# Optimization experiments

Hardware: AMD Instinct MI355X
Metric: run time of the kernel (lower is better)

## Reference

```python
import jax, jax.numpy as jnp
import numpy as np

N = 100000   # nodes
E = 1200000  # edges
D = 64       # feat_dim == num_hidden
G = 64       # graphs in batch
EPS = 1e-5   # BatchNorm eps


def setup_inputs() -> dict:
    key = jax.random.key(0)
    ks = jax.random.split(key, 24)
    inp = {}
    inp['x'] = jax.random.normal(ks[0], (N, D), jnp.float32)
    inp['edge_index'] = jax.random.randint(ks[1], (2, E), 0, N, dtype=jnp.int32)
    inp['batch'] = jnp.sort(jax.random.randint(ks[2], (N,), 0, G, dtype=jnp.int32))
    s = 1.0 / np.sqrt(D)
    for i, kw in zip(range(1, 4), ks[3:6]):
        inp[f'W{i}'] = jax.random.normal(kw, (D, D), jnp.float32) * s
    for i, kb in zip(range(1, 4), ks[6:9]):
        inp[f'b{i}'] = jax.random.normal(kb, (D,), jnp.float32) * 0.02
    for i, base in zip(range(1, 3), (9, 13)):
        inp[f'g{i}'] = 1.0 + 0.1 * jax.random.normal(ks[base], (D,), jnp.float32)
        inp[f'be{i}'] = 0.1 * jax.random.normal(ks[base + 1], (D,), jnp.float32)
        inp[f'rm{i}'] = 0.1 * jax.random.normal(ks[base + 2], (D,), jnp.float32)
        inp[f'rv{i}'] = jax.random.uniform(ks[base + 3], (D,), jnp.float32, 0.5, 1.5)
    return inp


def _gcn_conv(x, W, b, src, dst, n):
    # PyG GCNConv: h = X W; symmetric normalization with self-loops; scatter-add; + bias
    h = x @ W
    deg = jax.ops.segment_sum(jnp.ones((src.shape[0],), h.dtype), dst, num_segments=n) + 1.0
    dis = jax.lax.rsqrt(deg)                          # deg >= 1 from self loop
    msg = (dis[src] * dis[dst])[:, None] * h[src]     # [E, D] gather + normalize
    out = jax.ops.segment_sum(msg, dst, num_segments=n)
    out = out + (dis * dis)[:, None] * h              # self-loop contribution
    return out + b


def _bn(x, g, be, rm, rv):
    # BatchNorm1d in eval mode (running stats)
    return (x - rm) * jax.lax.rsqrt(rv + EPS) * g + be


def reference(x, edge_index, batch, W1, b1, W2, b2, W3, b3,
              g1, be1, rm1, rv1, g2, be2, rm2, rv2):
    src, dst = edge_index[0], edge_index[1]
    h = jax.nn.relu(_bn(_gcn_conv(x, W1, b1, src, dst, N), g1, be1, rm1, rv1))
    h = jax.nn.relu(_bn(_gcn_conv(h, W2, b2, src, dst, N), g2, be2, rm2, rv2))
    h = _gcn_conv(h, W3, b3, src, dst, N)
    # global mean pool over graphs
    counts = jax.ops.segment_sum(jnp.ones((N,), h.dtype), batch, num_segments=G)
    sums = jax.ops.segment_sum(h, batch, num_segments=G)
    hg = sums / jnp.maximum(counts, 1.0)[:, None]
    return (h, hg)
```

## Files before the change

### kernel.cpp

```cpp
#include <hip/hip_runtime.h>
#include <hip/hip_fp16.h>

#define D 64
#define EPS 1e-5f

#define BK_SHIFT 9
#define BK_W 512
#define NBMAX 256
#define BK_CAP 8192
#define CHUNK 4096

typedef _Float16 h8v __attribute__((ext_vector_type(8)));
typedef float f4v __attribute__((ext_vector_type(4)));


__global__ __launch_bounds__(256) void bucket_k(const int* __restrict__ src,
                                                const int* __restrict__ dst,
                                                int* __restrict__ bcnt,
                                                int* __restrict__ pairs,
                                                int e, int nbk) {
  __shared__ int hcnt[NBMAX];
  __shared__ int hbase[NBMAX];
  const int t = threadIdx.x;
  const int e0 = blockIdx.x * CHUNK;
  const int e1 = min(e0 + CHUNK, e);
  for (int i = t; i < nbk; i += 256) hcnt[i] = 0;
  __syncthreads();
  for (int i = e0 + t; i < e1; i += 256)
    atomicAdd(&hcnt[dst[i] >> BK_SHIFT], 1);
  __syncthreads();
  for (int i = t; i < nbk; i += 256) {
    int c = hcnt[i];
    hbase[i] = c ? atomicAdd(&bcnt[i], c) : 0;
    hcnt[i] = 0;
  }
  __syncthreads();
  for (int i = e0 + t; i < e1; i += 256) {
    int s = src[i], d = dst[i];
    int b = d >> BK_SHIFT;
    int r = hbase[b] + atomicAdd(&hcnt[b], 1);
    if (r < BK_CAP) pairs[(size_t)b * BK_CAP + r] = (s << BK_SHIFT) | (d & (BK_W - 1));
  }
}


__global__ __launch_bounds__(256) void bucket2csr_k(const int* __restrict__ bcnt,
                                                    const int* __restrict__ pairs,
                                                    int2* __restrict__ rpdeg,
                                                    float* __restrict__ dis,
                                                    int* __restrict__ col, int n) {
  __shared__ int h[BK_W];
  __shared__ int cur[BK_W];
  __shared__ int s1[256], s2[256];
  __shared__ int stage[BK_CAP];
  const int b = blockIdx.x, t = threadIdx.x;
  const int base = b << BK_SHIFT;
  const int slab0 = b * BK_CAP;
  const int m = min(bcnt[b], BK_CAP);

  h[t] = 0; h[t + 256] = 0;
  for (int i = t; i < BK_CAP; i += 256) stage[i] = 0;
  __syncthreads();
  const int* p = pairs + (size_t)b * BK_CAP;
  for (int i = t; i < m; i += 256) atomicAdd(&h[p[i] & (BK_W - 1)], 1);
  __syncthreads();

  const int pc1 = (h[t] + 3) & ~3;
  const int pc2 = (h[t + 256] + 3) & ~3;
  s1[t] = pc1; s2[t] = pc2;
  __syncthreads();
  for (int off = 1; off < 256; off <<= 1) {
    int x1 = (t >= off) ? s1[t - off] : 0;
    int x2 = (t >= off) ? s2[t - off] : 0;
    __syncthreads();
    s1[t] += x1; s2[t] += x2;
    __syncthreads();
  }
  const int tot1 = s1[255];
  const int mpad = tot1 + s2[255];
  cur[t]       = s1[t] - pc1;
  cur[t + 256] = tot1 + s2[t] - pc2;
  {
    int n1 = base + t, n2 = base + t + 256;
    if (n1 < n) { rpdeg[n1] = make_int2(slab0 + cur[t], h[t]);
                  dis[n1] = rsqrtf((float)h[t] + 1.0f); }
    if (n2 < n) { rpdeg[n2] = make_int2(slab0 + cur[t + 256], h[t + 256]);
                  dis[n2] = rsqrtf((float)h[t + 256] + 1.0f); }
  }
  __syncthreads();

  for (int i = t; i < m; i += 256) {
    int pk = p[i];
    int r = atomicAdd(&cur[pk & (BK_W - 1)], 1);
    stage[r] = pk >> BK_SHIFT;
  }
  __syncthreads();
  const int mout = min(mpad + 16, BK_CAP);
  for (int i = t; i < mout; i += 256) col[slab0 + i] = stage[i];
}


__global__ __launch_bounds__(256) void setup_k(const float* __restrict__ W1,
                                               const float* __restrict__ W2,
                                               const float* __restrict__ W3,
                                               const float* __restrict__ b1,
                                               const float* __restrict__ b2,
                                               const float* __restrict__ b3,
                                               const float* __restrict__ g1, const float* __restrict__ be1,
                                               const float* __restrict__ rm1, const float* __restrict__ rv1,
                                               const float* __restrict__ g2, const float* __restrict__ be2,
                                               const float* __restrict__ rm2, const float* __restrict__ rv2,
                                               _Float16* __restrict__ Wt1,
                                               _Float16* __restrict__ Wt2,
                                               _Float16* __restrict__ Wt3,
                                               float* __restrict__ scsh,
                                               int* __restrict__ zbase, int zwords,
                                               unsigned int* __restrict__ hzrowA,
                                               unsigned int* __restrict__ hzrowB) {
  int gid = blockIdx.x * 256 + threadIdx.x;
  if (gid < zwords) { zbase[gid] = 0; return; }
  gid -= zwords;
  if (gid < 64) {
    if (gid < 32) hzrowA[gid] = 0u; else hzrowB[gid - 32] = 0u;
    return;
  }
  gid -= 64;
  if (gid < 192) {
    int j = gid & 63, l = gid >> 6;
    float sc, sh;
    if (l == 0)      { sc = g1[j] * rsqrtf(rv1[j] + EPS); sh = (b1[j] - rm1[j]) * sc + be1[j]; }
    else if (l == 1) { sc = g2[j] * rsqrtf(rv2[j] + EPS); sh = (b2[j] - rm2[j]) * sc + be2[j]; }
    else             { sc = 1.0f;                          sh = b3[j]; }
    scsh[l * 128 + j] = sc;
    scsh[l * 128 + 64 + j] = sh;
    return;
  }
  gid -= 192;
  if (gid < 3 * 4096) {
    const int mat = gid >> 12, e = gid & 4095;
    const float* Wm = (mat == 0) ? W1 : (mat == 1) ? W2 : W3;
    _Float16* Wt    = (mat == 0) ? Wt1 : (mat == 1) ? Wt2 : Wt3;
    const int k = e >> 6, j = e & 63;
    Wt[j * 64 + k] = (_Float16)Wm[e];
  }
}


template <typename InT>
__global__ __launch_bounds__(256) void gemm_k(const InT* __restrict__ in,
                                              const _Float16* __restrict__ Wt,
                                              const float* __restrict__ dis,
                                              __half* __restrict__ out, int nrows) {
  const int lane = threadIdx.x & 63;
  const int w    = threadIdx.x >> 6;
  const int t16  = lane & 15;
  const int q    = lane >> 4;
  const int rb   = blockIdx.x * 64 + w * 16;
  if (rb >= nrows) return;

  h8v bf[4][2];
#pragma unroll
  for (int cg = 0; cg < 4; ++cg) {
    const _Float16* wp = Wt + (cg * 16 + t16) * 64 + q * 8;
    bf[cg][0] = *(const h8v*)(wp);
    bf[cg][1] = *(const h8v*)(wp + 32);
  }

  const int ar = min(rb + t16, nrows - 1);
  h8v a0, a1;
  if constexpr (sizeof(InT) == 2) {
    const _Float16* ap = (const _Float16*)in + (size_t)ar * D + q * 8;
    a0 = *(const h8v*)(ap);
    a1 = *(const h8v*)(ap + 32);
  } else {
    const float* ap = (const float*)in + (size_t)ar * D + q * 8;
    const float4 l0 = *(const float4*)(ap);
    const float4 h0 = *(const float4*)(ap + 4);
    const float4 l1 = *(const float4*)(ap + 32);
    const float4 h1 = *(const float4*)(ap + 36);
    a0[0] = (_Float16)l0.x; a0[1] = (_Float16)l0.y; a0[2] = (_Float16)l0.z; a0[3] = (_Float16)l0.w;
    a0[4] = (_Float16)h0.x; a0[5] = (_Float16)h0.y; a0[6] = (_Float16)h0.z; a0[7] = (_Float16)h0.w;
    a1[0] = (_Float16)l1.x; a1[1] = (_Float16)l1.y; a1[2] = (_Float16)l1.z; a1[3] = (_Float16)l1.w;
    a1[4] = (_Float16)h1.x; a1[5] = (_Float16)h1.y; a1[6] = (_Float16)h1.z; a1[7] = (_Float16)h1.w;
  }

  f4v acc0 = {0.f, 0.f, 0.f, 0.f};
  f4v acc1 = acc0, acc2 = acc0, acc3 = acc0;
  acc0 = __builtin_amdgcn_mfma_f32_16x16x32_f16(a0, bf[0][0], acc0, 0, 0, 0);
  acc1 = __builtin_amdgcn_mfma_f32_16x16x32_f16(a0, bf[1][0], acc1, 0, 0, 0);
  acc2 = __builtin_amdgcn_mfma_f32_16x16x32_f16(a0, bf[2][0], acc2, 0, 0, 0);
  acc3 = __builtin_amdgcn_mfma_f32_16x16x32_f16(a0, bf[3][0], acc3, 0, 0, 0);
  acc0 = __builtin_amdgcn_mfma_f32_16x16x32_f16(a1, bf[0][1], acc0, 0, 0, 0);
  acc1 = __builtin_amdgcn_mfma_f32_16x16x32_f16(a1, bf[1][1], acc1, 0, 0, 0);
  acc2 = __builtin_amdgcn_mfma_f32_16x16x32_f16(a1, bf[2][1], acc2, 0, 0, 0);
  acc3 = __builtin_amdgcn_mfma_f32_16x16x32_f16(a1, bf[3][1], acc3, 0, 0, 0);

  const float4 dv = *(const float4*)&dis[rb + q * 4];
  _Float16* oh = (_Float16*)out;
#pragma unroll
  for (int r = 0; r < 4; ++r) {
    const int row = rb + q * 4 + r;
    if (row < nrows) {
      const float dsc = (&dv.x)[r];
      _Float16* op = oh + (size_t)row * D + t16;
      op[0]  = (_Float16)(dsc * acc0[r]);
      op[16] = (_Float16)(dsc * acc1[r]);
      op[32] = (_Float16)(dsc * acc2[r]);
      op[48] = (_Float16)(dsc * acc3[r]);
    }
  }
}


template <bool RELU, typename OutT>
__global__ __launch_bounds__(256) void agg_k(const __half* __restrict__ h2s,
                                             const int2* __restrict__ rpdeg,
                                             const int* __restrict__ col,
                                             const float* __restrict__ dis,
                                             const float* __restrict__ scsh,
                                             OutT* __restrict__ out, int n) {
  const int lane = threadIdx.x & 63;
  const int wv   = (blockIdx.x * blockDim.x + threadIdx.x) >> 6;
  const int nb   = __builtin_amdgcn_readfirstlane(wv * 4);
  if (nb >= n) return;
  const int g  = lane >> 4;
  const int sl = lane & 15;
  const int jb = 4 * g;
  const uint2* __restrict__ h2v = (const uint2*)h2s;

  int nd[4], p[4], dg[4];
#pragma unroll
  for (int i = 0; i < 4; ++i) nd[i] = min(nb + i, n - 1);
#pragma unroll
  for (int i = 0; i < 4; ++i) { int2 rd = rpdeg[nd[i]]; p[i] = rd.x; dg[i] = rd.y; }

  uint2 self[4];
  int4  cc[4];
#pragma unroll
  for (int i = 0; i < 4; ++i) {
    self[i] = h2v[(size_t)nd[i] * 16 + sl];
    cc[i]   = *(const int4*)&col[p[i] + jb];
  }

  const __half2 zero2 = __floats2half2_rn(0.f, 0.f);
  const uint2 zz = make_uint2(0u, 0u);
  __half2 acc[4][4];
#pragma unroll
  for (int i = 0; i < 4; ++i)
#pragma unroll
    for (int s = 0; s < 4; ++s) acc[i][s] = zero2;

#pragma unroll
  for (int i = 0; i < 4; ++i) {
    uint2 r0 = h2v[(size_t)cc[i].x * 16 + sl];
    uint2 r1 = h2v[(size_t)cc[i].y * 16 + sl];
    uint2 r2 = h2v[(size_t)cc[i].z * 16 + sl];
    uint2 r3 = h2v[(size_t)cc[i].w * 16 + sl];
    r0 = (jb + 0 < dg[i]) ? r0 : zz;  r1 = (jb + 1 < dg[i]) ? r1 : zz;
    r2 = (jb + 2 < dg[i]) ? r2 : zz;  r3 = (jb + 3 < dg[i]) ? r3 : zz;
    acc[i][0] = __hadd2(acc[i][0], *(const __half2*)&r0.x);
    acc[i][1] = __hadd2(acc[i][1], *(const __half2*)&r0.y);
    acc[i][2] = __hadd2(acc[i][2], *(const __half2*)&r1.x);
    acc[i][3] = __hadd2(acc[i][3], *(const __half2*)&r1.y);
    acc[i][0] = __hadd2(acc[i][0], *(const __half2*)&r2.x);
    acc[i][1] = __hadd2(acc[i][1], *(const __half2*)&r2.y);
    acc[i][2] = __hadd2(acc[i][2], *(const __half2*)&r3.x);
    acc[i][3] = __hadd2(acc[i][3], *(const __half2*)&r3.y);
  }

#pragma unroll
  for (int i = 0; i < 4; ++i) {
    for (int e = 16; e < dg[i]; e += 16) {
      const int4 c2 = *(const int4*)&col[p[i] + e + jb];
      uint2 r0 = h2v[(size_t)c2.x * 16 + sl];
      uint2 r1 = h2v[(size_t)c2.y * 16 + sl];
      uint2 r2 = h2v[(size_t)c2.z * 16 + sl];
      uint2 r3 = h2v[(size_t)c2.w * 16 + sl];
      const int j = e + jb;
      r0 = (j + 0 < dg[i]) ? r0 : zz;  r1 = (j + 1 < dg[i]) ? r1 : zz;
      r2 = (j + 2 < dg[i]) ? r2 : zz;  r3 = (j + 3 < dg[i]) ? r3 : zz;
      acc[i][0] = __hadd2(acc[i][0], *(const __half2*)&r0.x);
      acc[i][1] = __hadd2(acc[i][1], *(const __half2*)&r0.y);
      acc[i][2] = __hadd2(acc[i][2], *(const __half2*)&r1.x);
      acc[i][3] = __hadd2(acc[i][3], *(const __half2*)&r1.y);
      acc[i][0] = __hadd2(acc[i][0], *(const __half2*)&r2.x);
      acc[i][1] = __hadd2(acc[i][1], *(const __half2*)&r2.y);
      acc[i][2] = __hadd2(acc[i][2], *(const __half2*)&r3.x);
      acc[i][3] = __hadd2(acc[i][3], *(const __half2*)&r3.y);
    }
  }

  const float4 sc = *(const float4*)&scsh[4 * sl];
  const float4 sh = *(const float4*)&scsh[64 + 4 * sl];

#pragma unroll
  for (int i = 0; i < 4; ++i) {
    const float2 a0 = __half22float2(acc[i][0]);
    const float2 a1 = __half22float2(acc[i][1]);
    const float2 a2 = __half22float2(acc[i][2]);
    const float2 a3 = __half22float2(acc[i][3]);
    const float2 s0f = __half22float2(*(const __half2*)&self[i].x);
    const float2 s1f = __half22float2(*(const __half2*)&self[i].y);
    float r0 = (a0.x + a2.x) + (g == 0 ? s0f.x : 0.f);
    float r1 = (a0.y + a2.y) + (g == 0 ? s0f.y : 0.f);
    float r2 = (a1.x + a3.x) + (g == 0 ? s1f.x : 0.f);
    float r3 = (a1.y + a3.y) + (g == 0 ? s1f.y : 0.f);
    r0 += __shfl_xor(r0, 16, 64); r1 += __shfl_xor(r1, 16, 64);
    r2 += __shfl_xor(r2, 16, 64); r3 += __shfl_xor(r3, 16, 64);
    r0 += __shfl_xor(r0, 32, 64); r1 += __shfl_xor(r1, 32, 64);
    r2 += __shfl_xor(r2, 32, 64); r3 += __shfl_xor(r3, 32, 64);
    const float di = dis[nd[i]];
    float o0 = fmaf(di * r0, sc.x, sh.x);
    float o1 = fmaf(di * r1, sc.y, sh.y);
    float o2 = fmaf(di * r2, sc.z, sh.z);
    float o3 = fmaf(di * r3, sc.w, sh.w);
    if (RELU) {
      o0 = fmaxf(o0, 0.f); o1 = fmaxf(o1, 0.f);
      o2 = fmaxf(o2, 0.f); o3 = fmaxf(o3, 0.f);
    }
    if (g == 0 && nb + i < n) {
      if constexpr (sizeof(OutT) == 2) {
        union { __half2 h[2]; uint2 u; } v;
        v.h[0] = __floats2half2_rn(o0, o1);
        v.h[1] = __floats2half2_rn(o2, o3);
        *(uint2*)&out[(size_t)nd[i] * D + 4 * sl] = v.u;
      } else {
        *(float4*)&out[(size_t)nd[i] * D + 4 * sl] = make_float4(o0, o1, o2, o3);
      }
    }
  }
}


template <bool RELU>
__global__ __launch_bounds__(256) void aggemm_k(const __half* __restrict__ h2s,
                                                const int2* __restrict__ rpdeg,
                                                const int* __restrict__ col,
                                                const float* __restrict__ dis,
                                                const float* __restrict__ scsh,
                                                const _Float16* __restrict__ Wt,
                                                __half* __restrict__ out, int n) {
  __shared__ _Float16 ylds[16][72];
  const int lane = threadIdx.x & 63;
  const int w    = threadIdx.x >> 6;
  const int nb   = __builtin_amdgcn_readfirstlane(blockIdx.x * 16 + w * 4);
  const int g  = lane >> 4;
  const int sl = lane & 15;
  const int jb = 4 * g;
  const uint2* __restrict__ h2v = (const uint2*)h2s;

  int nd[4], p[4], dg[4];
#pragma unroll
  for (int i = 0; i < 4; ++i) nd[i] = min(nb + i, n - 1);
#pragma unroll
  for (int i = 0; i < 4; ++i) { int2 rd = rpdeg[nd[i]]; p[i] = rd.x; dg[i] = rd.y; }

  uint2 self[4];
  int4  cc[4];
#pragma unroll
  for (int i = 0; i < 4; ++i) {
    self[i] = h2v[(size_t)nd[i] * 16 + sl];
    cc[i]   = *(const int4*)&col[p[i] + jb];
  }

  const __half2 zero2 = __floats2half2_rn(0.f, 0.f);
  const uint2 zz = make_uint2(0u, 0u);
  __half2 acc[4][4];
#pragma unroll
  for (int i = 0; i < 4; ++i)
#pragma unroll
    for (int s = 0; s < 4; ++s) acc[i][s] = zero2;

#pragma unroll
  for (int i = 0; i < 4; ++i) {
    uint2 r0 = h2v[(size_t)cc[i].x * 16 + sl];
    uint2 r1 = h2v[(size_t)cc[i].y * 16 + sl];
    uint2 r2 = h2v[(size_t)cc[i].z * 16 + sl];
    uint2 r3 = h2v[(size_t)cc[i].w * 16 + sl];
    r0 = (jb + 0 < dg[i]) ? r0 : zz;  r1 = (jb + 1 < dg[i]) ? r1 : zz;
    r2 = (jb + 2 < dg[i]) ? r2 : zz;  r3 = (jb + 3 < dg[i]) ? r3 : zz;
    acc[i][0] = __hadd2(acc[i][0], *(const __half2*)&r0.x);
    acc[i][1] = __hadd2(acc[i][1], *(const __half2*)&r0.y);
    acc[i][2] = __hadd2(acc[i][2], *(const __half2*)&r1.x);
    acc[i][3] = __hadd2(acc[i][3], *(const __half2*)&r1.y);
    acc[i][0] = __hadd2(acc[i][0], *(const __half2*)&r2.x);
    acc[i][1] = __hadd2(acc[i][1], *(const __half2*)&r2.y);
    acc[i][2] = __hadd2(acc[i][2], *(const __half2*)&r3.x);
    acc[i][3] = __hadd2(acc[i][3], *(const __half2*)&r3.y);
  }

#pragma unroll
  for (int i = 0; i < 4; ++i) {
    for (int e = 16; e < dg[i]; e += 16) {
      const int4 c2 = *(const int4*)&col[p[i] + e + jb];
      uint2 r0 = h2v[(size_t)c2.x * 16 + sl];
      uint2 r1 = h2v[(size_t)c2.y * 16 + sl];
      uint2 r2 = h2v[(size_t)c2.z * 16 + sl];
      uint2 r3 = h2v[(size_t)c2.w * 16 + sl];
      const int j = e + jb;
      r0 = (j + 0 < dg[i]) ? r0 : zz;  r1 = (j + 1 < dg[i]) ? r1 : zz;
      r2 = (j + 2 < dg[i]) ? r2 : zz;  r3 = (j + 3 < dg[i]) ? r3 : zz;
      acc[i][0] = __hadd2(acc[i][0], *(const __half2*)&r0.x);
      acc[i][1] = __hadd2(acc[i][1], *(const __half2*)&r0.y);
      acc[i][2] = __hadd2(acc[i][2], *(const __half2*)&r1.x);
      acc[i][3] = __hadd2(acc[i][3], *(const __half2*)&r1.y);
      acc[i][0] = __hadd2(acc[i][0], *(const __half2*)&r2.x);
      acc[i][1] = __hadd2(acc[i][1], *(const __half2*)&r2.y);
      acc[i][2] = __hadd2(acc[i][2], *(const __half2*)&r3.x);
      acc[i][3] = __hadd2(acc[i][3], *(const __half2*)&r3.y);
    }
  }

  const float4 sc = *(const float4*)&scsh[4 * sl];
  const float4 sh = *(const float4*)&scsh[64 + 4 * sl];

#pragma unroll
  for (int i = 0; i < 4; ++i) {
    const float2 a0 = __half22float2(acc[i][0]);
    const float2 a1 = __half22float2(acc[i][1]);
    const float2 a2 = __half22float2(acc[i][2]);
    const float2 a3 = __half22float2(acc[i][3]);
    const float2 s0f = __half22float2(*(const __half2*)&self[i].x);
    const float2 s1f = __half22float2(*(const __half2*)&self[i].y);
    float r0 = (a0.x + a2.x) + (g == 0 ? s0f.x : 0.f);
    float r1 = (a0.y + a2.y) + (g == 0 ? s0f.y : 0.f);
    float r2 = (a1.x + a3.x) + (g == 0 ? s1f.x : 0.f);
    float r3 = (a1.y + a3.y) + (g == 0 ? s1f.y : 0.f);
    r0 += __shfl_xor(r0, 16, 64); r1 += __shfl_xor(r1, 16, 64);
    r2 += __shfl_xor(r2, 16, 64); r3 += __shfl_xor(r3, 16, 64);
    r0 += __shfl_xor(r0, 32, 64); r1 += __shfl_xor(r1, 32, 64);
    r2 += __shfl_xor(r2, 32, 64); r3 += __shfl_xor(r3, 32, 64);
    const float di = dis[nd[i]];
    float o0 = fmaf(di * r0, sc.x, sh.x);
    float o1 = fmaf(di * r1, sc.y, sh.y);
    float o2 = fmaf(di * r2, sc.z, sh.z);
    float o3 = fmaf(di * r3, sc.w, sh.w);
    if (RELU) {
      o0 = fmaxf(o0, 0.f); o1 = fmaxf(o1, 0.f);
      o2 = fmaxf(o2, 0.f); o3 = fmaxf(o3, 0.f);
    }
    if (g == 0) {
      union { __half2 h[2]; uint2 u; } v;
      v.h[0] = __floats2half2_rn(o0, o1);
      v.h[1] = __floats2half2_rn(o2, o3);
      *(uint2*)&ylds[w * 4 + i][4 * sl] = v.u;
    }
  }

  __syncthreads();

  {
    const h8v a0 = *(const h8v*)&ylds[sl][g * 8];
    const h8v a1 = *(const h8v*)&ylds[sl][g * 8 + 32];
    const _Float16* wp = Wt + (w * 16 + sl) * 64 + g * 8;
    const h8v b0 = *(const h8v*)(wp);
    const h8v b1 = *(const h8v*)(wp + 32);
    f4v ga = {0.f, 0.f, 0.f, 0.f};
    ga = __builtin_amdgcn_mfma_f32_16x16x32_f16(a0, b0, ga, 0, 0, 0);
    ga = __builtin_amdgcn_mfma_f32_16x16x32_f16(a1, b1, ga, 0, 0, 0);

    const int rb = blockIdx.x * 16;
    const float4 dv = *(const float4*)&dis[rb + g * 4];
    _Float16* oh = (_Float16*)out;
#pragma unroll
    for (int r = 0; r < 4; ++r) {
      const int row = rb + g * 4 + r;
      if (row < n) {
        const float dsc = (&dv.x)[r];
        oh[(size_t)row * D + w * 16 + sl] = (_Float16)(dsc * ga[r]);
      }
    }
  }
}


__global__ __launch_bounds__(256) void pool_k(const float* __restrict__ h,
                                              const int* __restrict__ batch,
                                              float* __restrict__ psum,
                                              float* __restrict__ pcnt, int n) {
  int lane  = threadIdx.x & 63;
  int wid   = __builtin_amdgcn_readfirstlane((blockIdx.x * blockDim.x + threadIdx.x) >> 6);
  int start = wid * 64;
  if (start >= n) return;
  int end = min(start + 64, n);
  int cur = batch[start];
  float sum = 0.f;
  int run = 0;
  for (int i = start; i < end; ++i) {
    int g = batch[i];
    if (g != cur) {
      atomicAdd(&psum[cur * D + lane], sum);
      if (lane == 0) atomicAdd(&pcnt[cur], (float)run);
      sum = 0.f; run = 0; cur = g;
    }
    sum += h[(size_t)i * D + lane];
    run += 1;
  }
  atomicAdd(&psum[cur * D + lane], sum);
  if (lane == 0) atomicAdd(&pcnt[cur], (float)run);
}

__global__ void pooldiv_k(const float* __restrict__ psum, const float* __restrict__ pcnt,
                          float* __restrict__ hg) {
  int t = blockIdx.x * blockDim.x + threadIdx.x;
  if (t < 64 * D) hg[t] = psum[t] / fmaxf(pcnt[t >> 6], 1.0f);
}


extern "C" void kernel_launch(void* const* d_in, const int* in_sizes, int n_in,
                              void* d_out, int out_size, void* d_ws, size_t ws_size,
                              hipStream_t stream) {
  const float* x   = (const float*)d_in[0];
  const int*   ei  = (const int*)d_in[1];
  const int*   bat = (const int*)d_in[2];
  const float* W1  = (const float*)d_in[3];
  const float* W2  = (const float*)d_in[4];
  const float* W3  = (const float*)d_in[5];
  const float* b1  = (const float*)d_in[6];
  const float* b2  = (const float*)d_in[7];
  const float* b3  = (const float*)d_in[8];
  const float* g1  = (const float*)d_in[9];
  const float* be1 = (const float*)d_in[10];
  const float* rm1 = (const float*)d_in[11];
  const float* rv1 = (const float*)d_in[12];
  const float* g2  = (const float*)d_in[13];
  const float* be2 = (const float*)d_in[14];
  const float* rm2 = (const float*)d_in[15];
  const float* rv2 = (const float*)d_in[16];

  const int n = in_sizes[0] / D;
  const int e = in_sizes[1] / 2;
  const int* src = ei;
  const int* dst = ei + e;
  const int nbk = (n + BK_W - 1) >> BK_SHIFT;

  char* ws = (char*)d_ws;
  size_t off = 0;
  auto alloc = [&](size_t bytes) -> void* {
    void* p = ws + off;
    off = (off + bytes + 255) & ~(size_t)255;
    return p;
  };
  __half*   hbufB = (__half*)alloc((size_t)(n + 1) * D * 2);
  int*      pairs = (int*)alloc((size_t)NBMAX * BK_CAP * 4);
  __half*   hbufA = (__half*)alloc((size_t)(n + 1) * D * 2);
  int2*     rpdeg = (int2*)alloc((size_t)(n + 1) * 8);
  float*    dis   = (float*)alloc((size_t)(n + 16) * 4);
  int*      col   = (int*)alloc((size_t)NBMAX * BK_CAP * 4);
  float*    scsh  = (float*)alloc(6 * 64 * 4);
  _Float16* Wt1   = (_Float16*)alloc(4096 * 2);
  _Float16* Wt2   = (_Float16*)alloc(4096 * 2);
  _Float16* Wt3   = (_Float16*)alloc(4096 * 2);
  int*      bcnt  = (int*)alloc(NBMAX * 4);
  float*    psum  = (float*)alloc(64 * D * 4);
  float*    pcnt  = (float*)alloc(64 * 4);
  const int zwords = (int)((((char*)pcnt + 64 * 4) - (char*)bcnt) / 4);

  float* hout = (float*)d_out;
  float* hg   = (float*)d_out + (size_t)n * D;

  const int setup_items = zwords + 64 + 192 + 3 * 4096;
  setup_k<<<(setup_items + 255) / 256, 256, 0, stream>>>(
      W1, W2, W3, b1, b2, b3, g1, be1, rm1, rv1, g2, be2, rm2, rv2,
      Wt1, Wt2, Wt3, scsh, bcnt, zwords,
      (unsigned int*)(hbufA + (size_t)n * D),
      (unsigned int*)(hbufB + (size_t)n * D));

  bucket_k<<<(e + CHUNK - 1) / CHUNK, 256, 0, stream>>>(src, dst, bcnt, pairs, e, nbk);
  bucket2csr_k<<<nbk, 256, 0, stream>>>(bcnt, pairs, rpdeg, dis, col, n);

  const int gemm_blocks = (n + 63) / 64;
  const int fuse_blocks = (n + 15) / 16;
  const int agg_waves   = (n + 3) / 4;
  const int agg_blocks  = (agg_waves * 64 + 255) / 256;

  gemm_k<float><<<gemm_blocks, 256, 0, stream>>>(x, Wt1, dis, hbufA, n);
  aggemm_k<true><<<fuse_blocks, 256, 0, stream>>>(hbufA, rpdeg, col, dis, scsh + 0 * 128, Wt2, hbufB, n);
  aggemm_k<true><<<fuse_blocks, 256, 0, stream>>>(hbufB, rpdeg, col, dis, scsh + 1 * 128, Wt3, hbufA, n);
  agg_k<false, float><<<agg_blocks, 256, 0, stream>>>(hbufA, rpdeg, col, dis, scsh + 2 * 128, hout, n);

  const int pool_waves = (n + 63) / 64;
  pool_k<<<(pool_waves * 64 + 255) / 256, 256, 0, stream>>>(hout, bat, psum, pcnt, n);
  pooldiv_k<<<(64 * D + 255) / 256, 256, 0, stream>>>(psum, pcnt, hg);
}
```

Baseline: 278.7 us.

## Fuse mean-pool into last aggregation and widen per-wave node tiles to eight

The final aggregation kernel now also does the global mean-pool partial sums, accumulating per-graph runs in registers and flushing them with atomics. This removes the separate pool kernel and its re-read of the fp32 output. Both aggregation kernels now process eight nodes per wave instead of four, with 32-row MFMA tiles in the fused agg+GEMM kernel and self-row loads deferred until after the gather. The wider tiles add memory-level parallelism and amortize loads, but raise register pressure, which may lower occupancy.

Measured after the change: 337.7 us. 1.21x slower.

```diff
diff --git a/kernel.cpp b/kernel.cpp
--- a/kernel.cpp
+++ b/kernel.cpp
@@ -212,46 +212,44 @@
 }
 
 
-template <bool RELU, typename OutT>
-__global__ __launch_bounds__(256) void agg_k(const __half* __restrict__ h2s,
-                                             const int2* __restrict__ rpdeg,
-                                             const int* __restrict__ col,
-                                             const float* __restrict__ dis,
-                                             const float* __restrict__ scsh,
-                                             OutT* __restrict__ out, int n) {
+
+template <bool RELU>
+__global__ __launch_bounds__(256) void aggemm_k(const __half* __restrict__ h2s,
+                                                const int2* __restrict__ rpdeg,
+                                                const int* __restrict__ col,
+                                                const float* __restrict__ dis,
+                                                const float* __restrict__ scsh,
+                                                const _Float16* __restrict__ Wt,
+                                                __half* __restrict__ out, int n) {
+  __shared__ _Float16 ylds[32][72];
   const int lane = threadIdx.x & 63;
-  const int wv   = (blockIdx.x * blockDim.x + threadIdx.x) >> 6;
-  const int nb   = __builtin_amdgcn_readfirstlane(wv * 4);
-  if (nb >= n) return;
+  const int w    = threadIdx.x >> 6;
+  const int nb   = __builtin_amdgcn_readfirstlane(blockIdx.x * 32 + w * 8);
   const int g  = lane >> 4;
   const int sl = lane & 15;
   const int jb = 4 * g;
   const uint2* __restrict__ h2v = (const uint2*)h2s;
 
-  int nd[4], p[4], dg[4];
-#pragma unroll
-  for (int i = 0; i < 4; ++i) nd[i] = min(nb + i, n - 1);
-#pragma unroll
-  for (int i = 0; i < 4; ++i) { int2 rd = rpdeg[nd[i]]; p[i] = rd.x; dg[i] = rd.y; }
-
-  uint2 self[4];
-  int4  cc[4];
-#pragma unroll
-  for (int i = 0; i < 4; ++i) {
-    self[i] = h2v[(size_t)nd[i] * 16 + sl];
-    cc[i]   = *(const int4*)&col[p[i] + jb];
-  }
+  int nd[8], p[8], dg[8];
+#pragma unroll
+  for (int i = 0; i < 8; ++i) nd[i] = min(nb + i, n - 1);
+#pragma unroll
+  for (int i = 0; i < 8; ++i) { int2 rd = rpdeg[nd[i]]; p[i] = rd.x; dg[i] = rd.y; }
+
+  int4 cc[8];
+#pragma unroll
+  for (int i = 0; i < 8; ++i) cc[i] = *(const int4*)&col[p[i] + jb];
 
   const __half2 zero2 = __floats2half2_rn(0.f, 0.f);
   const uint2 zz = make_uint2(0u, 0u);
-  __half2 acc[4][4];
-#pragma unroll
-  for (int i = 0; i < 4; ++i)
+  __half2 acc[8][4];
+#pragma unroll
+  for (int i = 0; i < 8; ++i)
 #pragma unroll
     for (int s = 0; s < 4; ++s) acc[i][s] = zero2;
 
 #pragma unroll
-  for (int i = 0; i < 4; ++i) {
+  for (int i = 0; i < 8; ++i) {
     uint2 r0 = h2v[(size_t)cc[i].x * 16 + sl];
     uint2 r1 = h2v[(size_t)cc[i].y * 16 + sl];
     uint2 r2 = h2v[(size_t)cc[i].z * 16 + sl];
@@ -269,7 +267,7 @@
   }
 
 #pragma unroll
-  for (int i = 0; i < 4; ++i) {
+  for (int i = 0; i < 8; ++i) {
     for (int e = 16; e < dg[i]; e += 16) {
       const int4 c2 = *(const int4*)&col[p[i] + e + jb];
       uint2 r0 = h2v[(size_t)c2.x * 16 + sl];
@@ -290,11 +288,15 @@
     }
   }
 
+  uint2 self[8];
+#pragma unroll
+  for (int i = 0; i < 8; ++i) self[i] = h2v[(size_t)nd[i] * 16 + sl];
+
   const float4 sc = *(const float4*)&scsh[4 * sl];
   const float4 sh = *(const float4*)&scsh[64 + 4 * sl];
 
 #pragma unroll
-  for (int i = 0; i < 4; ++i) {
+  for (int i = 0; i < 8; ++i) {
     const float2 a0 = __half22float2(acc[i][0]);
     const float2 a1 = __half22float2(acc[i][1]);
     const float2 a2 = __half22float2(acc[i][2]);
@@ -318,61 +320,84 @@
       o0 = fmaxf(o0, 0.f); o1 = fmaxf(o1, 0.f);
       o2 = fmaxf(o2, 0.f); o3 = fmaxf(o3, 0.f);
     }
-    if (g == 0 && nb + i < n) {
-      if constexpr (sizeof(OutT) == 2) {
-        union { __half2 h[2]; uint2 u; } v;
-        v.h[0] = __floats2half2_rn(o0, o1);
-        v.h[1] = __floats2half2_rn(o2, o3);
-        *(uint2*)&out[(size_t)nd[i] * D + 4 * sl] = v.u;
-      } else {
-        *(float4*)&out[(size_t)nd[i] * D + 4 * sl] = make_float4(o0, o1, o2, o3);
-      }
-    }
-  }
-}
-
-
-template <bool RELU>
-__global__ __launch_bounds__(256) void aggemm_k(const __half* __restrict__ h2s,
-                                                const int2* __restrict__ rpdeg,
-                                                const int* __restrict__ col,
-                                                const float* __restrict__ dis,
-                                                const float* __restrict__ scsh,
-                                                const _Float16* __restrict__ Wt,
-                                                __half* __restrict__ out, int n) {
-  __shared__ _Float16 ylds[16][72];
+    if (g == 0) {
+      union { __half2 h[2]; uint2 u; } v;
+      v.h[0] = __floats2half2_rn(o0, o1);
+      v.h[1] = __floats2half2_rn(o2, o3);
+      *(uint2*)&ylds[w * 8 + i][4 * sl] = v.u;
+    }
+  }
+
+  __syncthreads();
+
+  {
+    const h8v a0t0 = *(const h8v*)&ylds[sl][g * 8];
+    const h8v a1t0 = *(const h8v*)&ylds[sl][g * 8 + 32];
+    const h8v a0t1 = *(const h8v*)&ylds[16 + sl][g * 8];
+    const h8v a1t1 = *(const h8v*)&ylds[16 + sl][g * 8 + 32];
+    const _Float16* wp = Wt + (w * 16 + sl) * 64 + g * 8;
+    const h8v b0 = *(const h8v*)(wp);
+    const h8v b1 = *(const h8v*)(wp + 32);
+    f4v ga0 = {0.f, 0.f, 0.f, 0.f};
+    f4v ga1 = ga0;
+    ga0 = __builtin_amdgcn_mfma_f32_16x16x32_f16(a0t0, b0, ga0, 0, 0, 0);
+    ga0 = __builtin_amdgcn_mfma_f32_16x16x32_f16(a1t0, b1, ga0, 0, 0, 0);
+    ga1 = __builtin_amdgcn_mfma_f32_16x16x32_f16(a0t1, b0, ga1, 0, 0, 0);
+    ga1 = __builtin_amdgcn_mfma_f32_16x16x32_f16(a1t1, b1, ga1, 0, 0, 0);
+
+    const int rb = blockIdx.x * 32;
+    const float4 dv0 = *(const float4*)&dis[rb + g * 4];
+    const float4 dv1 = *(const float4*)&dis[rb + 16 + g * 4];
+    _Float16* oh = (_Float16*)out;
+#pragma unroll
+    for (int r = 0; r < 4; ++r) {
+      const int row0 = rb + g * 4 + r;
+      if (row0 < n) oh[(size_t)row0 * D + w * 16 + sl] = (_Float16)((&dv0.x)[r] * ga0[r]);
+      const int row1 = rb + 16 + g * 4 + r;
+      if (row1 < n) oh[(size_t)row1 * D + w * 16 + sl] = (_Float16)((&dv1.x)[r] * ga1[r]);
+    }
+  }
+}
+
+
+__global__ __launch_bounds__(256) void aggpool_k(const __half* __restrict__ h2s,
+                                                 const int2* __restrict__ rpdeg,
+                                                 const int* __restrict__ col,
+                                                 const float* __restrict__ dis,
+                                                 const float* __restrict__ scsh,
+                                                 const int* __restrict__ batch,
+                                                 float* __restrict__ out,
+                                                 float* __restrict__ psum,
+                                                 float* __restrict__ pcnt, int n) {
   const int lane = threadIdx.x & 63;
-  const int w    = threadIdx.x >> 6;
-  const int nb   = __builtin_amdgcn_readfirstlane(blockIdx.x * 16 + w * 4);
+  const int wv   = (blockIdx.x * blockDim.x + threadIdx.x) >> 6;
+  const int nb   = __builtin_amdgcn_readfirstlane(wv * 8);
+  if (nb >= n) return;
   const int g  = lane >> 4;
   const int sl = lane & 15;
   const int jb = 4 * g;
   const uint2* __restrict__ h2v = (const uint2*)h2s;
 
-  int nd[4], p[4], dg[4];
-#pragma unroll
-  for (int i = 0; i < 4; ++i) nd[i] = min(nb + i, n - 1);
-#pragma unroll
-  for (int i = 0; i < 4; ++i) { int2 rd = rpdeg[nd[i]]; p[i] = rd.x; dg[i] = rd.y; }
-
-  uint2 self[4];
-  int4  cc[4];
-#pragma unroll
-  for (int i = 0; i < 4; ++i) {
-    self[i] = h2v[(size_t)nd[i] * 16 + sl];
-    cc[i]   = *(const int4*)&col[p[i] + jb];
-  }
+  int nd[8], p[8], dg[8];
+#pragma unroll
+  for (int i = 0; i < 8; ++i) nd[i] = min(nb + i, n - 1);
+#pragma unroll
+  for (int i = 0; i < 8; ++i) { int2 rd = rpdeg[nd[i]]; p[i] = rd.x; dg[i] = rd.y; }
+
+  int4 cc[8];
+#pragma unroll
+  for (int i = 0; i < 8; ++i) cc[i] = *(const int4*)&col[p[i] + jb];
 
   const __half2 zero2 = __floats2half2_rn(0.f, 0.f);
   const uint2 zz = make_uint2(0u, 0u);
-  __half2 acc[4][4];
-#pragma unroll
-  for (int i = 0; i < 4; ++i)
+  __half2 acc[8][4];
+#pragma unroll
+  for (int i = 0; i < 8; ++i)
 #pragma unroll
     for (int s = 0; s < 4; ++s) acc[i][s] = zero2;
 
 #pragma unroll
-  for (int i = 0; i < 4; ++i) {
+  for (int i = 0; i < 8; ++i) {
     uint2 r0 = h2v[(size_t)cc[i].x * 16 + sl];
     uint2 r1 = h2v[(size_t)cc[i].y * 16 + sl];
     uint2 r2 = h2v[(size_t)cc[i].z * 16 + sl];
@@ -390,7 +415,7 @@
   }
 
 #pragma unroll
-  for (int i = 0; i < 4; ++i) {
+  for (int i = 0; i < 8; ++i) {
     for (int e = 16; e < dg[i]; e += 16) {
       const int4 c2 = *(const int4*)&col[p[i] + e + jb];
       uint2 r0 = h2v[(size_t)c2.x * 16 + sl];
@@ -411,11 +436,22 @@
     }
   }
 
+  uint2 self[8];
+#pragma unroll
+  for (int i = 0; i < 8; ++i) self[i] = h2v[(size_t)nd[i] * 16 + sl];
+
+  int bt[8];
+#pragma unroll
+  for (int i = 0; i < 8; ++i) bt[i] = batch[nd[i]];
+
   const float4 sc = *(const float4*)&scsh[4 * sl];
   const float4 sh = *(const float4*)&scsh[64 + 4 * sl];
 
-#pragma unroll
-  for (int i = 0; i < 4; ++i) {
+  float ps0 = 0.f, ps1 = 0.f, ps2 = 0.f, ps3 = 0.f;
+  int cur = bt[0], run = 0;
+
+#pragma unroll
+  for (int i = 0; i < 8; ++i) {
     const float2 a0 = __half22float2(acc[i][0]);
     const float2 a1 = __half22float2(acc[i][1]);
     const float2 a2 = __half22float2(acc[i][2]);
@@ -431,73 +467,33 @@
     r0 += __shfl_xor(r0, 32, 64); r1 += __shfl_xor(r1, 32, 64);
     r2 += __shfl_xor(r2, 32, 64); r3 += __shfl_xor(r3, 32, 64);
     const float di = dis[nd[i]];
-    float o0 = fmaf(di * r0, sc.x, sh.x);
-    float o1 = fmaf(di * r1, sc.y, sh.y);
-    float o2 = fmaf(di * r2, sc.z, sh.z);
-    float o3 = fmaf(di * r3, sc.w, sh.w);
-    if (RELU) {
-      o0 = fmaxf(o0, 0.f); o1 = fmaxf(o1, 0.f);
-      o2 = fmaxf(o2, 0.f); o3 = fmaxf(o3, 0.f);
-    }
-    if (g == 0) {
-      union { __half2 h[2]; uint2 u; } v;
-      v.h[0] = __floats2half2_rn(o0, o1);
-      v.h[1] = __floats2half2_rn(o2, o3);
-      *(uint2*)&ylds[w * 4 + i][4 * sl] = v.u;
-    }
-  }
-
-  __syncthreads();
-
-  {
-    const h8v a0 = *(const h8v*)&ylds[sl][g * 8];
-    const h8v a1 = *(const h8v*)&ylds[sl][g * 8 + 32];
-    const _Float16* wp = Wt + (w * 16 + sl) * 64 + g * 8;
-    const h8v b0 = *(const h8v*)(wp);
-    const h8v b1 = *(const h8v*)(wp + 32);
-    f4v ga = {0.f, 0.f, 0.f, 0.f};
-    ga = __builtin_amdgcn_mfma_f32_16x16x32_f16(a0, b0, ga, 0, 0, 0);
-    ga = __builtin_amdgcn_mfma_f32_16x16x32_f16(a1, b1, ga, 0, 0, 0);
-
-    const int rb = blockIdx.x * 16;
-    const float4 dv = *(const float4*)&dis[rb + g * 4];
-    _Float16* oh = (_Float16*)out;
-#pragma unroll
-    for (int r = 0; r < 4; ++r) {
-      const int row = rb + g * 4 + r;
-      if (row < n) {
-        const float dsc = (&dv.x)[r];
-        oh[(size_t)row * D + w * 16 + sl] = (_Float16)(dsc * ga[r]);
+    const float o0 = fmaf(di * r0, sc.x, sh.x);
+    const float o1 = fmaf(di * r1, sc.y, sh.y);
+    const float o2 = fmaf(di * r2, sc.z, sh.z);
+    const float o3 = fmaf(di * r3, sc.w, sh.w);
+    const bool valid = (nb + i < n);
+    if (g == 0 && valid) {
+      *(float4*)&out[(size_t)nd[i] * D + 4 * sl] = make_float4(o0, o1, o2, o3);
+    }
+    if (bt[i] != cur) {
+      if (g == 0) {
+        atomicAdd(&psum[cur * D + 4 * sl + 0], ps0);
+        atomicAdd(&psum[cur * D + 4 * sl + 1], ps1);
+        atomicAdd(&psum[cur * D + 4 * sl + 2], ps2);
+        atomicAdd(&psum[cur * D + 4 * sl + 3], ps3);
+        if (lane == 0) atomicAdd(&pcnt[cur], (float)run);
       }
-    }
-  }
-}
-
-
-__global__ __launch_bounds__(256) void pool_k(const float* __restrict__ h,
-                                              const int* __restrict__ batch,
-                                              float* __restrict__ psum,
-                                              float* __restrict__ pcnt, int n) {
-  int lane  = threadIdx.x & 63;
-  int wid   = __builtin_amdgcn_readfirstlane((blockIdx.x * blockDim.x + threadIdx.x) >> 6);
-  int start = wid * 64;
-  if (start >= n) return;
-  int end = min(start + 64, n);
-  int cur = batch[start];
-  float sum = 0.f;
-  int run = 0;
-  for (int i = start; i < end; ++i) {
-    int g = batch[i];
-    if (g != cur) {
-      atomicAdd(&psum[cur * D + lane], sum);
-      if (lane == 0) atomicAdd(&pcnt[cur], (float)run);
-      sum = 0.f; run = 0; cur = g;
-    }
-    sum += h[(size_t)i * D + lane];
-    run += 1;
-  }
-  atomicAdd(&psum[cur * D + lane], sum);
-  if (lane == 0) atomicAdd(&pcnt[cur], (float)run);
+      ps0 = ps1 = ps2 = ps3 = 0.f; run = 0; cur = bt[i];
+    }
+    if (valid) { ps0 += o0; ps1 += o1; ps2 += o2; ps3 += o3; run += 1; }
+  }
+  if (g == 0 && run > 0) {
+    atomicAdd(&psum[cur * D + 4 * sl + 0], ps0);
+    atomicAdd(&psum[cur * D + 4 * sl + 1], ps1);
+    atomicAdd(&psum[cur * D + 4 * sl + 2], ps2);
+    atomicAdd(&psum[cur * D + 4 * sl + 3], ps3);
+    if (lane == 0) atomicAdd(&pcnt[cur], (float)run);
+  }
 }
 
 __global__ void pooldiv_k(const float* __restrict__ psum, const float* __restrict__ pcnt,
@@ -545,7 +541,7 @@
   int*      pairs = (int*)alloc((size_t)NBMAX * BK_CAP * 4);
   __half*   hbufA = (__half*)alloc((size_t)(n + 1) * D * 2);
   int2*     rpdeg = (int2*)alloc((size_t)(n + 1) * 8);
-  float*    dis   = (float*)alloc((size_t)(n + 16) * 4);
+  float*    dis   = (float*)alloc((size_t)(n + 32) * 4);
   int*      col   = (int*)alloc((size_t)NBMAX * BK_CAP * 4);
   float*    scsh  = (float*)alloc(6 * 64 * 4);
   _Float16* Wt1   = (_Float16*)alloc(4096 * 2);
@@ -570,16 +566,14 @@
   bucket2csr_k<<<nbk, 256, 0, stream>>>(bcnt, pairs, rpdeg, dis, col, n);
 
   const int gemm_blocks = (n + 63) / 64;
-  const int fuse_blocks = (n + 15) / 16;
-  const int agg_waves   = (n + 3) / 4;
+  const int fuse_blocks = (n + 31) / 32;
+  const int agg_waves   = (n + 7) / 8;
   const int agg_blocks  = (agg_waves * 64 + 255) / 256;
 
   gemm_k<float><<<gemm_blocks, 256, 0, stream>>>(x, Wt1, dis, hbufA, n);
   aggemm_k<true><<<fuse_blocks, 256, 0, stream>>>(hbufA, rpdeg, col, dis, scsh + 0 * 128, Wt2, hbufB, n);
   aggemm_k<true><<<fuse_blocks, 256, 0, stream>>>(hbufB, rpdeg, col, dis, scsh + 1 * 128, Wt3, hbufA, n);
-  agg_k<false, float><<<agg_blocks, 256, 0, stream>>>(hbufA, rpdeg, col, dis, scsh + 2 * 128, hout, n);
-
-  const int pool_waves = (n + 63) / 64;
-  pool_k<<<(pool_waves * 64 + 255) / 256, 256, 0, stream>>>(hout, bat, psum, pcnt, n);
+  aggpool_k<<<agg_blocks, 256, 0, stream>>>(hbufA, rpdeg, col, dis, scsh + 2 * 128, bat,
+                                            hout, psum, pcnt, n);
   pooldiv_k<<<(64 * D + 255) / 256, 256, 0, stream>>>(psum, pcnt, hg);
 }
```
